# Kernel tuning notes

Measured on AMD Instinct MI355X. Metric: run time of the kernel, lower is better.

## Reference

```python
import jax, jax.numpy as jnp
import numpy as np

N = 50000        # nodes
E = 1_600_000    # edges
IN = 64          # in_channels
HID = 16         # hidden_dim (per-head channels)
HEADS = 8
OUT = 32         # out_channels
B = 256          # graphs in batch
NEG_SLOPE = 0.2  # PyG GATv2Conv default


def gatv2_conv(x, edge_index, wl, bl, wr, br, att, bias, heads, ch, concat, num_nodes):
    """Faithful GATv2Conv (PyG semantics, eval mode, add self-loops disabled upstream
    is not the case in PyG default, but the module uses default add_self_loops=True;
    we add them here)."""
    src, dst = edge_index[0], edge_index[1]
    # PyG default add_self_loops=True
    loop = jnp.arange(num_nodes, dtype=src.dtype)
    src = jnp.concatenate([src, loop])
    dst = jnp.concatenate([dst, loop])
    xl = (x @ wl + bl).reshape(num_nodes, heads, ch)  # source transform
    xr = (x @ wr + br).reshape(num_nodes, heads, ch)  # target transform
    # per-edge GATv2 score: att . leaky_relu(xl[src] + xr[dst])
    e = jax.nn.leaky_relu(xl[src] + xr[dst], NEG_SLOPE)          # [E, H, C]
    logits = jnp.einsum('ehc,hc->eh', e, att)                     # [E, H]
    # segment softmax over incoming edges of each dst node (max detached, as in PyG)
    m = jax.lax.stop_gradient(jax.ops.segment_max(logits, dst, num_segments=num_nodes))
    a = jnp.exp(logits - m[dst])
    denom = jax.ops.segment_sum(a, dst, num_segments=num_nodes)
    alpha = a / (denom[dst] + 1e-16)                              # [E, H]
    msg = xl[src] * alpha[..., None]                              # [E, H, C]
    out = jax.ops.segment_sum(msg, dst, num_segments=num_nodes)   # [N, H, C]
    if concat:
        out = out.reshape(num_nodes, heads * ch) + bias
    else:
        out = out.mean(axis=1) + bias
    return out


def global_mean_pool(x, batch, num_graphs):
    s = jax.ops.segment_sum(x, batch, num_segments=num_graphs)
    cnt = jax.ops.segment_sum(jnp.ones((x.shape[0],), x.dtype), batch, num_segments=num_graphs)
    return s / jnp.maximum(cnt, 1.0)[:, None]


def setup_inputs() -> dict:
    key = jax.random.key(0)
    ks = jax.random.split(key, 24)
    f32 = jnp.float32
    def g(k, shape, s=0.1):
        return jax.random.normal(k, shape, f32) * s
    inp = {
        'x': jax.random.normal(ks[0], (N, IN), f32),
        'edge_index': jax.random.randint(ks[1], (2, E), 0, N, dtype=jnp.int32),
        'batch': jnp.sort(jax.random.randint(ks[2], (N,), 0, B, dtype=jnp.int32)),
        # conv1: GATv2Conv(IN -> HID, heads=HEADS, concat=True)
        'wl1': g(ks[3], (IN, HEADS * HID)), 'bl1': jnp.zeros((HEADS * HID,), f32),
        'wr1': g(ks[4], (IN, HEADS * HID)), 'br1': jnp.zeros((HEADS * HID,), f32),
        'att1': g(ks[5], (HEADS, HID)),
        'bias1': jnp.zeros((HEADS * HID,), f32),
        # conv2: GATv2Conv(HEADS*HID -> HID, heads=1, concat=False)
        'wl2': g(ks[6], (HEADS * HID, HID)), 'bl2': jnp.zeros((HID,), f32),
        'wr2': g(ks[7], (HEADS * HID, HID)), 'br2': jnp.zeros((HID,), f32),
        'att2': g(ks[8], (1, HID)),
        'bias2': jnp.zeros((HID,), f32),
        # MLP: HID -> 2*HID -> HID -> OUT
        'w_m1': g(ks[9], (HID, 2 * HID)), 'b_m1': jnp.zeros((2 * HID,), f32),
        'w_m2': g(ks[10], (2 * HID, HID)), 'b_m2': jnp.zeros((HID,), f32),
        'w_m3': g(ks[11], (HID, OUT)), 'b_m3': jnp.zeros((OUT,), f32),
    }
    return inp


def reference(x, edge_index, batch,
              wl1, bl1, wr1, br1, att1, bias1,
              wl2, bl2, wr2, br2, att2, bias2,
              w_m1, b_m1, w_m2, b_m2, w_m3, b_m3):
    # eval mode: all dropouts are identity
    h = jax.nn.elu(gatv2_conv(x, edge_index, wl1, bl1, wr1, br1, att1, bias1,
                              HEADS, HID, True, N))
    h = jax.nn.elu(gatv2_conv(h, edge_index, wl2, bl2, wr2, br2, att2, bias2,
                              1, HID, False, N))
    h = global_mean_pool(h, batch, B)                 # [B, HID]
    h = jax.nn.elu(h @ w_m1 + b_m1)
    h = jax.nn.elu(h @ w_m2 + b_m2)
    return h @ w_m3 + b_m3                            # [B, OUT]
```

## Files before the change

kernel.cpp:

```cpp
#include <hip/hip_runtime.h>
#include <hip/hip_bf16.h>
#include <hip/hip_fp16.h>
#include <math.h>

#define NN   50000
#define NE   1600000
#define EP   (NE + NN)
#define NB   256
#define BK_SH 6
#define BKN  (1 << BK_SH)
#define NBKT ((NN + BKN - 1) >> BK_SH)
#define CAP_SH 12
#define CAP  (1 << CAP_SH)
#define ET   32
#define EB   (256 * ET)
#define EBLK ((NE + EB - 1) / EB)
#define G1   ((NN + 31) / 32)

__device__ __forceinline__ float elu_f(float x)   { return x > 0.0f ? x : expm1f(x); }
__device__ __forceinline__ float lrelu_f(float x) { return fmaxf(x, 0.2f * x); }

__global__ __launch_bounds__(256) void k_gemm1_bucket(
    const float* __restrict__ x, const float* __restrict__ wl,
    const float* __restrict__ bl, const float* __restrict__ wr,
    const float* __restrict__ br, __half* __restrict__ xl1, float* __restrict__ xr1,
    const int* __restrict__ ei, int* __restrict__ bcursor,
    unsigned int* __restrict__ bb)
{
    __shared__ float xs[32 * 64];
    __shared__ int lh[NBKT];
    __shared__ int cur[NBKT];
    const int tid = threadIdx.x;

    if (blockIdx.x < G1) {
        const int n0  = blockIdx.x * 32;
        const int nrem = min(32, NN - n0);

        const float4* xg = (const float4*)(x + (size_t)n0 * 64);
        float4* xs4 = (float4*)xs;
        const int lim4 = nrem * 16;
        for (int i = tid; i < lim4; i += 256) xs4[i] = xg[i];
        __syncthreads();

        const int g  = tid >> 6;
        const int c0 = (tid & 63) * 4;
        const bool isl = (c0 < 128);
        const float* w  = isl ? wl : wr;
        const float* b  = isl ? bl : br;
        const int    cw = isl ? c0 : (c0 - 128);

        float4 acc[8];
#pragma unroll
        for (int r = 0; r < 8; ++r) acc[r] = make_float4(0.f, 0.f, 0.f, 0.f);

        for (int k4 = 0; k4 < 16; ++k4) {
            const float4 w0 = *(const float4*)&w[(k4*4+0)*128 + cw];
            const float4 w1 = *(const float4*)&w[(k4*4+1)*128 + cw];
            const float4 w2 = *(const float4*)&w[(k4*4+2)*128 + cw];
            const float4 w3 = *(const float4*)&w[(k4*4+3)*128 + cw];
#pragma unroll
            for (int r = 0; r < 8; ++r) {
                const float4 xv = xs4[(g*8+r)*16 + k4];
                acc[r].x += xv.x*w0.x + xv.y*w1.x + xv.z*w2.x + xv.w*w3.x;
                acc[r].y += xv.x*w0.y + xv.y*w1.y + xv.z*w2.y + xv.w*w3.y;
                acc[r].z += xv.x*w0.z + xv.y*w1.z + xv.z*w2.z + xv.w*w3.z;
                acc[r].w += xv.x*w0.w + xv.y*w1.w + xv.z*w2.w + xv.w*w3.w;
            }
        }
        const float4 bv = *(const float4*)&b[cw];
#pragma unroll
        for (int r = 0; r < 8; ++r) {
            const int row = g*8 + r;
            if (row < nrem) {
                float4 o = make_float4(acc[r].x + bv.x, acc[r].y + bv.y,
                                       acc[r].z + bv.z, acc[r].w + bv.w);
                if (isl) {
                    __half2* dst = (__half2*)&xl1[(size_t)(n0 + row) * 128 + cw];
                    dst[0] = __floats2half2_rn(o.x, o.y);
                    dst[1] = __floats2half2_rn(o.z, o.w);
                } else {
                    *(float4*)&xr1[(size_t)(n0 + row) * 128 + cw] = o;
                }
            }
        }
    } else {
        const int bid = blockIdx.x - G1;
        for (int i = tid; i < NBKT; i += 256) lh[i] = 0;
        __syncthreads();

        const int t = bid * 256 + tid;
        const bool act = (t * ET < NE);
        int4 dreg[ET / 4];
        if (act) {
            const int4* dp = (const int4*)&ei[NE + t * ET];
#pragma unroll
            for (int q = 0; q < ET / 4; ++q) {
                dreg[q] = dp[q];
                atomicAdd(&lh[dreg[q].x >> BK_SH], 1);
                atomicAdd(&lh[dreg[q].y >> BK_SH], 1);
                atomicAdd(&lh[dreg[q].z >> BK_SH], 1);
                atomicAdd(&lh[dreg[q].w >> BK_SH], 1);
            }
        }
        __syncthreads();
        for (int i = tid; i < NBKT; i += 256) {
            int h = lh[i];
            if (h > 0) cur[i] = atomicAdd(&bcursor[i], h);
        }
        __syncthreads();
        if (act) {
            const int4* sp = (const int4*)&ei[t * ET];
#pragma unroll
            for (int q = 0; q < ET / 4; ++q) {
                int4 s = sp[q];
                int4 d = dreg[q];
                int bkt, p;
                bkt = d.x >> BK_SH; p = atomicAdd(&cur[bkt], 1);
                if (p < ((bkt + 1) << CAP_SH))
                    bb[p] = ((unsigned)(d.x & (BKN-1)) << 17) | (unsigned)s.x;
                bkt = d.y >> BK_SH; p = atomicAdd(&cur[bkt], 1);
                if (p < ((bkt + 1) << CAP_SH))
                    bb[p] = ((unsigned)(d.y & (BKN-1)) << 17) | (unsigned)s.y;
                bkt = d.z >> BK_SH; p = atomicAdd(&cur[bkt], 1);
                if (p < ((bkt + 1) << CAP_SH))
                    bb[p] = ((unsigned)(d.z & (BKN-1)) << 17) | (unsigned)s.z;
                bkt = d.w >> BK_SH; p = atomicAdd(&cur[bkt], 1);
                if (p < ((bkt + 1) << CAP_SH))
                    bb[p] = ((unsigned)(d.w & (BKN-1)) << 17) | (unsigned)s.w;
            }
        }
    }
}

__global__ void k_binit(int* __restrict__ bcursor)
{
    int i = blockIdx.x * 256 + threadIdx.x;
    if (i < NBKT) bcursor[i] = i << CAP_SH;
}

__global__ __launch_bounds__(256) void k_bfinal(
    const unsigned int* __restrict__ bb, const int* __restrict__ bcursor,
    int* __restrict__ rowp, int* __restrict__ slist)
{
    __shared__ int cnt[BKN], cur[BKN];
    __shared__ int red[256];
    const int b = blockIdx.x, tid = threadIdx.x;
    const int db0 = b << BK_SH;
    const int dn  = min(BKN, NN - db0);

    int part = 0;
    for (int i = tid; i < b; i += 256)
        part += min(bcursor[i] - (i << CAP_SH), CAP);
    red[tid] = part;
    __syncthreads();
    for (int ofs = 128; ofs >= 1; ofs >>= 1) {
        if (tid < ofs) red[tid] += red[tid + ofs];
        __syncthreads();
    }
    const int ebeg = red[0];
    const int count = min(bcursor[b] - (b << CAP_SH), CAP);
    const unsigned int* src = bb + ((size_t)b << CAP_SH);
    const int out0 = ebeg + db0;

    int c0 = 0;
    if (tid < BKN) {
        c0 = (tid < dn) ? 1 : 0;
        cnt[tid] = c0;
    }
    __syncthreads();
    for (int i = tid; i < count; i += 256)
        atomicAdd(&cnt[src[i] >> 17], 1);
    __syncthreads();
    if (tid < BKN) c0 = cnt[tid];
    for (int ofs = 1; ofs < BKN; ofs <<= 1) {
        int v = 0;
        if (tid < BKN && tid >= ofs) v = cnt[tid - ofs];
        __syncthreads();
        if (tid < BKN) cnt[tid] += v;
        __syncthreads();
    }
    if (tid < BKN) {
        int ex = cnt[tid] - c0;
        cur[tid] = ex + 1;
        if (tid < dn) {
            rowp[db0 + tid] = out0 + ex;
            slist[out0 + ex] = db0 + tid;
        }
    }
    if (b == 0 && tid == 0) rowp[NN] = EP;
    __syncthreads();
    for (int i = tid; i < count; i += 256) {
        unsigned u = src[i];
        int p = atomicAdd(&cur[u >> 17], 1);
        slist[out0 + p] = (int)(u & 0x1FFFFu);
    }
}

__global__ __launch_bounds__(256) void k_conv1_agg(
    const __half* __restrict__ xl1, const float* __restrict__ xr1,
    const float* __restrict__ att, const float* __restrict__ bias1,
    const int* __restrict__ rowp, const int* __restrict__ slist,
    float* __restrict__ h1)
{
    const int d = (blockIdx.x * 256 + threadIdx.x) >> 6;
    if (d >= NN) return;
    const int lane = threadIdx.x & 63;
    const int h = lane >> 3, e = lane & 7;
    const int cb = h * 16;

    float xrv[16], atv[16];
    {
        const float4* xrp = (const float4*)&xr1[(size_t)d * 128 + cb];
        const float4* atp = (const float4*)&att[cb];
#pragma unroll
        for (int q = 0; q < 4; ++q) {
            float4 a4 = xrp[q];
            xrv[q*4+0] = a4.x; xrv[q*4+1] = a4.y; xrv[q*4+2] = a4.z; xrv[q*4+3] = a4.w;
            float4 b4 = atp[q];
            atv[q*4+0] = b4.x; atv[q*4+1] = b4.y; atv[q*4+2] = b4.z; atv[q*4+3] = b4.w;
        }
    }

    const int beg = rowp[d], end = rowp[d + 1];

    float den = 0.f;
    float a[16];
#pragma unroll
    for (int c = 0; c < 16; ++c) a[c] = 0.f;

    for (int base = beg; base < end; base += 64) {
        const int nb = min(64, end - base);
        int sv = (lane < nb) ? slist[base + lane] : 0;
        for (int c8 = 0; c8 * 8 < nb; c8 += 2) {
            const int idx0 = c8 * 8 + e;
            const int idx1 = idx0 + 8;
            const int s0 = __shfl(sv, idx0);
            const int s1 = __shfl(sv, idx1 & 63);
            const bool e0 = (idx0 < nb), e1 = (idx1 < nb);
            float4 p0, p1, q0, q1;
            if (e0) {
                const float4* vp = (const float4*)(xl1 + (size_t)s0 * 128 + cb);
                p0 = vp[0]; p1 = vp[1];
            }
            if (e1) {
                const float4* vp = (const float4*)(xl1 + (size_t)s1 * 128 + cb);
                q0 = vp[0]; q1 = vp[1];
            }
            if (e0) {
                float v[16];
                const __half2* hh = (const __half2*)&p0;
#pragma unroll
                for (int q = 0; q < 4; ++q) {
                    float2 f = __half22float2(hh[q]);
                    v[2*q] = f.x; v[2*q+1] = f.y;
                }
                const __half2* hg = (const __half2*)&p1;
#pragma unroll
                for (int q = 0; q < 4; ++q) {
                    float2 f = __half22float2(hg[q]);
                    v[8+2*q] = f.x; v[9+2*q] = f.y;
                }
                float s = 0.f;
#pragma unroll
                for (int c = 0; c < 16; ++c) s += atv[c] * lrelu_f(v[c] + xrv[c]);
                const float w = __expf(fminf(s, 80.f));
                den += w;
#pragma unroll
                for (int c = 0; c < 16; ++c) a[c] += w * v[c];
            }
            if (e1) {
                float v[16];
                const __half2* hh = (const __half2*)&q0;
#pragma unroll
                for (int q = 0; q < 4; ++q) {
                    float2 f = __half22float2(hh[q]);
                    v[2*q] = f.x; v[2*q+1] = f.y;
                }
                const __half2* hg = (const __half2*)&q1;
#pragma unroll
                for (int q = 0; q < 4; ++q) {
                    float2 f = __half22float2(hg[q]);
                    v[8+2*q] = f.x; v[9+2*q] = f.y;
                }
                float s = 0.f;
#pragma unroll
                for (int c = 0; c < 16; ++c) s += atv[c] * lrelu_f(v[c] + xrv[c]);
                const float w = __expf(fminf(s, 80.f));
                den += w;
#pragma unroll
                for (int c = 0; c < 16; ++c) a[c] += w * v[c];
            }
        }
    }

    den += __shfl_xor(den, 1);
    den += __shfl_xor(den, 2);
    den += __shfl_xor(den, 4);

    const bool b0 = (e & 1), b1 = (e & 2), b2 = (e & 4);
    float t1[8], u1[8];
#pragma unroll
    for (int j = 0; j < 8; ++j) {
        t1[j] = b0 ? a[j + 8] : a[j];
        u1[j] = b0 ? a[j] : a[j + 8];
    }
#pragma unroll
    for (int j = 0; j < 8; ++j) t1[j] += __shfl_xor(u1[j], 1);
    float t2[4], u2[4];
#pragma unroll
    for (int j = 0; j < 4; ++j) {
        t2[j] = b1 ? t1[j + 4] : t1[j];
        u2[j] = b1 ? t1[j] : t1[j + 4];
    }
#pragma unroll
    for (int j = 0; j < 4; ++j) t2[j] += __shfl_xor(u2[j], 2);
    float t3[2], u3[2];
#pragma unroll
    for (int j = 0; j < 2; ++j) {
        t3[j] = b2 ? t2[j + 2] : t2[j];
        u3[j] = b2 ? t2[j] : t2[j + 2];
    }
#pragma unroll
    for (int j = 0; j < 2; ++j) t3[j] += __shfl_xor(u3[j], 4);

    const int c0 = (b0 ? 8 : 0) + (b1 ? 4 : 0) + (b2 ? 2 : 0);
    const float inv = 1.0f / (den + 1e-16f);
    const int c = cb + c0;
    const float o0 = elu_f(t3[0] * inv + bias1[c]);
    const float o1 = elu_f(t3[1] * inv + bias1[c + 1]);
    *(float2*)&h1[(size_t)d * 128 + c] = make_float2(o0, o1);
}

__global__ __launch_bounds__(256) void k_gemm2(
    const float* __restrict__ h1, const float* __restrict__ wl,
    const float* __restrict__ bl, const float* __restrict__ wr,
    const float* __restrict__ br, __half* __restrict__ xl2, float* __restrict__ xr2)
{
    __shared__ float xs[32 * 132];
    const int tid = threadIdx.x;
    const int n0  = blockIdx.x * 32;
    const int nrem = min(32, NN - n0);

    for (int i = tid; i < nrem * 128; i += 256) {
        int row = i >> 7, col = i & 127;
        xs[row * 132 + col] = h1[(size_t)(n0 + row) * 128 + col];
    }
    __syncthreads();

    const int r  = tid >> 3;
    const int c0 = (tid & 7) * 4;
    const bool isl = (c0 < 16);
    const float* w = isl ? wl : wr;
    const float* b = isl ? bl : br;
    const int    c = isl ? c0 : (c0 - 16);

    float4 acc = make_float4(0.f, 0.f, 0.f, 0.f);
    for (int k4 = 0; k4 < 32; ++k4) {
        const float4 w0 = *(const float4*)&w[(k4*4+0)*16 + c];
        const float4 w1 = *(const float4*)&w[(k4*4+1)*16 + c];
        const float4 w2 = *(const float4*)&w[(k4*4+2)*16 + c];
        const float4 w3 = *(const float4*)&w[(k4*4+3)*16 + c];
        const float4 xv = *(const float4*)&xs[r * 132 + k4 * 4];
        acc.x += xv.x*w0.x + xv.y*w1.x + xv.z*w2.x + xv.w*w3.x;
        acc.y += xv.x*w0.y + xv.y*w1.y + xv.z*w2.y + xv.w*w3.y;
        acc.z += xv.x*w0.z + xv.y*w1.z + xv.z*w2.z + xv.w*w3.z;
        acc.w += xv.x*w0.w + xv.y*w1.w + xv.z*w2.w + xv.w*w3.w;
    }
    if (r < nrem) {
        const float4 bv = *(const float4*)&b[c];
        float4 o = make_float4(acc.x + bv.x, acc.y + bv.y, acc.z + bv.z, acc.w + bv.w);
        if (isl) {
            __half2* dst = (__half2*)&xl2[(size_t)(n0 + r) * 16 + c];
            dst[0] = __floats2half2_rn(o.x, o.y);
            dst[1] = __floats2half2_rn(o.z, o.w);
        } else {
            *(float4*)&xr2[(size_t)(n0 + r) * 16 + c] = o;
        }
    }
}

__global__ __launch_bounds__(256) void k_conv2_agg(
    const __half* __restrict__ xl2, const float* __restrict__ xr2,
    const float* __restrict__ att, const float* __restrict__ bias2,
    const int* __restrict__ rowp, const int* __restrict__ slist,
    float* __restrict__ h2)
{
    const int d = (blockIdx.x * 256 + threadIdx.x) >> 6;
    if (d >= NN) return;
    const int lane = threadIdx.x & 63;
    const int eq = lane >> 2, c4 = lane & 3;

    const float4 xr = *(const float4*)&xr2[(size_t)d * 16 + c4 * 4];
    const float4 at = *(const float4*)&att[c4 * 4];
    const int beg = rowp[d], end = rowp[d + 1];

    float den = 0.f;
    float4 acc = make_float4(0.f, 0.f, 0.f, 0.f);

    for (int base = beg; base < end; base += 64) {
        const int nb = min(64, end - base);
        int sv = (lane < nb) ? slist[base + lane] : 0;
        for (int c16 = 0; c16 * 16 < nb; c16 += 2) {
            const int idx0 = c16 * 16 + eq;
            const int idx1 = idx0 + 16;
            const int s0 = __shfl(sv, idx0 & 63);
            const int s1 = __shfl(sv, idx1 & 63);
            const bool ee0 = (idx0 < nb), ee1 = (idx1 < nb);
            float2 ra, rb;
            if (ee0) ra = *(const float2*)(xl2 + (size_t)s0 * 16 + c4 * 4);
            if (ee1) rb = *(const float2*)(xl2 + (size_t)s1 * 16 + c4 * 4);
            {
                const __half2* hp = (const __half2*)&ra;
                float2 f0 = make_float2(0.f, 0.f), f1 = f0;
                if (ee0) { f0 = __half22float2(hp[0]); f1 = __half22float2(hp[1]); }
                float pp = at.x * lrelu_f(f0.x + xr.x)
                         + at.y * lrelu_f(f0.y + xr.y)
                         + at.z * lrelu_f(f1.x + xr.z)
                         + at.w * lrelu_f(f1.y + xr.w);
                pp += __shfl_xor(pp, 1);
                pp += __shfl_xor(pp, 2);
                if (ee0) {
                    const float w = __expf(fminf(pp, 80.f));
                    den += w;
                    acc.x += w * f0.x;
                    acc.y += w * f0.y;
                    acc.z += w * f1.x;
                    acc.w += w * f1.y;
                }
            }
            {
                const __half2* hp = (const __half2*)&rb;
                float2 f0 = make_float2(0.f, 0.f), f1 = f0;
                if (ee1) { f0 = __half22float2(hp[0]); f1 = __half22float2(hp[1]); }
                float pp = at.x * lrelu_f(f0.x + xr.x)
                         + at.y * lrelu_f(f0.y + xr.y)
                         + at.z * lrelu_f(f1.x + xr.z)
                         + at.w * lrelu_f(f1.y + xr.w);
                pp += __shfl_xor(pp, 1);
                pp += __shfl_xor(pp, 2);
                if (ee1) {
                    const float w = __expf(fminf(pp, 80.f));
                    den += w;
                    acc.x += w * f0.x;
                    acc.y += w * f0.y;
                    acc.z += w * f1.x;
                    acc.w += w * f1.y;
                }
            }
        }
    }
#pragma unroll
    for (int ofs = 4; ofs < 64; ofs <<= 1) {
        den   += __shfl_xor(den, ofs);
        acc.x += __shfl_xor(acc.x, ofs);
        acc.y += __shfl_xor(acc.y, ofs);
        acc.z += __shfl_xor(acc.z, ofs);
        acc.w += __shfl_xor(acc.w, ofs);
    }
    if (eq == 0) {
        const float inv = 1.0f / (den + 1e-16f);
        const float4 bv = *(const float4*)&bias2[c4 * 4];
        float4 o;
        o.x = elu_f(acc.x * inv + bv.x);
        o.y = elu_f(acc.y * inv + bv.y);
        o.z = elu_f(acc.z * inv + bv.z);
        o.w = elu_f(acc.w * inv + bv.w);
        *(float4*)&h2[(size_t)d * 16 + c4 * 4] = o;
    }
}

__global__ __launch_bounds__(256) void k_pool(
    const float* __restrict__ h2, const int* __restrict__ batch,
    float* __restrict__ pooled, float* __restrict__ cnt)
{
    __shared__ int se[2];
    __shared__ float sm[256];
    const int b = blockIdx.x, tid = threadIdx.x;
    if (tid < 2) {
        int key = b + tid, lo = 0, hi = NN;
        while (lo < hi) {
            int mid = (lo + hi) >> 1;
            if (batch[mid] < key) lo = mid + 1; else hi = mid;
        }
        se[tid] = lo;
    }
    __syncthreads();
    const int s = se[0], e = se[1];
    const int c = tid & 15, slot = tid >> 4;
    float acc = 0.f;
    for (int n = s + slot; n < e; n += 16) acc += h2[(size_t)n * 16 + c];
    sm[tid] = acc;
    __syncthreads();
    for (int ofs = 128; ofs >= 16; ofs >>= 1) {
        if (tid < ofs) sm[tid] += sm[tid + ofs];
        __syncthreads();
    }
    if (tid < 16) pooled[b * 16 + tid] = sm[tid];
    if (tid == 16) cnt[b] = (float)(e - s);
}

__global__ __launch_bounds__(256) void k_mlp(
    const float* __restrict__ pooled, const float* __restrict__ cnt,
    const float* __restrict__ w1, const float* __restrict__ b1,
    const float* __restrict__ w2, const float* __restrict__ b2,
    const float* __restrict__ w3, const float* __restrict__ b3,
    float* __restrict__ out)
{
    __shared__ float w1s[16*32], w2s[32*16], w3s[16*32], b1s[32], b2s[16], b3s[32];
    const int tid = threadIdx.x;
    for (int i = tid; i < 512; i += 256) { w1s[i] = w1[i]; w2s[i] = w2[i]; w3s[i] = w3[i]; }
    if (tid < 32) b1s[tid] = b1[tid];
    if (tid < 16) b2s[tid] = b2[tid];
    if (tid < 32) b3s[tid] = b3[tid];
    __syncthreads();

    const int g = tid;
    const float inv = 1.0f / fmaxf(cnt[g], 1.0f);
    float hb[16];
#pragma unroll
    for (int k = 0; k < 16; ++k) hb[k] = pooled[g * 16 + k] * inv;

    float t1[32];
#pragma unroll
    for (int j = 0; j < 32; ++j) t1[j] = b1s[j];
    for (int k = 0; k < 16; ++k)
#pragma unroll
        for (int j = 0; j < 32; ++j) t1[j] += hb[k] * w1s[k * 32 + j];
#pragma unroll
    for (int j = 0; j < 32; ++j) t1[j] = elu_f(t1[j]);

    float t2[16];
#pragma unroll
    for (int j = 0; j < 16; ++j) t2[j] = b2s[j];
    for (int k = 0; k < 32; ++k)
#pragma unroll
        for (int j = 0; j < 16; ++j) t2[j] += t1[k] * w2s[k * 16 + j];
#pragma unroll
    for (int j = 0; j < 16; ++j) t2[j] = elu_f(t2[j]);

#pragma unroll
    for (int j = 0; j < 32; ++j) {
        float o = b3s[j];
        for (int k = 0; k < 16; ++k) o += t2[k] * w3s[k * 32 + j];
        out[g * 32 + j] = o;
    }
}

extern "C" void kernel_launch(void* const* d_in, const int* in_sizes, int n_in,
                              void* d_out, int out_size, void* d_ws, size_t ws_size,
                              hipStream_t stream)
{
    const float* x     = (const float*)d_in[0];
    const int*   ei    = (const int*)d_in[1];
    const int*   batch = (const int*)d_in[2];
    const float* wl1   = (const float*)d_in[3];
    const float* bl1   = (const float*)d_in[4];
    const float* wr1   = (const float*)d_in[5];
    const float* br1   = (const float*)d_in[6];
    const float* att1  = (const float*)d_in[7];
    const float* bias1 = (const float*)d_in[8];
    const float* wl2   = (const float*)d_in[9];
    const float* bl2   = (const float*)d_in[10];
    const float* wr2   = (const float*)d_in[11];
    const float* br2   = (const float*)d_in[12];
    const float* att2  = (const float*)d_in[13];
    const float* bias2 = (const float*)d_in[14];
    const float* wm1   = (const float*)d_in[15];
    const float* bm1   = (const float*)d_in[16];
    const float* wm2   = (const float*)d_in[17];
    const float* bm2   = (const float*)d_in[18];
    const float* wm3   = (const float*)d_in[19];
    const float* bm3   = (const float*)d_in[20];
    float* out = (float*)d_out;

    char* base = (char*)d_ws;
    size_t off = 0;
    auto alloc = [&](size_t bytes) -> void* {
        void* p = base + off;
        off += (bytes + 255) & ~(size_t)255;
        return p;
    };
    __half* xl1  = (__half*)alloc((size_t)NN * 128 * 2);
    float* xr1   = (float*)alloc((size_t)NN * 128 * 4);
    float* h1    = (float*)alloc((size_t)NN * 128 * 4);
    int*   slist = (int*)  alloc((size_t)EP * 4);
    unsigned int* bb = (unsigned int*)alloc((size_t)NBKT * CAP * 4);
    int*   rowp  = (int*)  alloc((size_t)(NN + 1) * 4);
    int*   bcursor=(int*)  alloc((size_t)NBKT * 4);
    __half* xl2  = (__half*)alloc((size_t)NN * 16 * 2);
    float* xr2   = (float*)alloc((size_t)NN * 16 * 4);
    float* h2    = (float*)alloc((size_t)NN * 16 * 4);
    float* pooled= (float*)alloc((size_t)NB * 16 * 4);
    float* cnt   = (float*)alloc((size_t)NB * 4);

    k_binit<<<(NBKT + 255) / 256, 256, 0, stream>>>(bcursor);
    k_gemm1_bucket<<<G1 + EBLK, 256, 0, stream>>>(x, wl1, bl1, wr1, br1, xl1, xr1,
                                                  ei, bcursor, bb);
    k_bfinal<<<NBKT, 256, 0, stream>>>(bb, bcursor, rowp, slist);
    k_conv1_agg<<<(NN * 64) / 256, 256, 0, stream>>>(xl1, xr1, att1, bias1, rowp, slist, h1);
    k_gemm2<<<(NN + 31) / 32, 256, 0, stream>>>(h1, wl2, bl2, wr2, br2, xl2, xr2);
    k_conv2_agg<<<(NN * 64) / 256, 256, 0, stream>>>(xl2, xr2, att2, bias2, rowp, slist, h2);
    k_pool<<<NB, 256, 0, stream>>>(h2, batch, pooled, cnt);
    k_mlp<<<1, 256, 0, stream>>>(pooled, cnt, wm1, bm1, wm2, bm2, wm3, bm3, out);
}
```

Before: 324.5 us.

## Fuse layer-2 linear transform into conv1 aggregation and simplify conv2 loop

Folds the second GATv2 layer's linear projections (wl2/wr2) into the conv1 aggregation kernel. Each block stages the combined 128x32 weight in shared memory and computes xl2/xr2 directly from the per-node h1 row kept in LDS. This removes the h1 buffer's global write and read-back and one kernel launch. The cost is a 16KB weight load into LDS per block (each block handles only 4 nodes) plus extra syncthreads, and the dropped `d >= NN` early return is harmless only because NN*64 divides evenly by 256. Separately, conv2's edge loop is de-unrolled from two edges per iteration to one, which may reduce memory-level parallelism.

```diff
diff --git a/kernel.cpp b/kernel.cpp
--- a/kernel.cpp
+++ b/kernel.cpp
@@ -200,11 +200,25 @@
     const __half* __restrict__ xl1, const float* __restrict__ xr1,
     const float* __restrict__ att, const float* __restrict__ bias1,
     const int* __restrict__ rowp, const int* __restrict__ slist,
-    float* __restrict__ h1)
-{
-    const int d = (blockIdx.x * 256 + threadIdx.x) >> 6;
-    if (d >= NN) return;
-    const int lane = threadIdx.x & 63;
+    const float* __restrict__ wl2, const float* __restrict__ bl2,
+    const float* __restrict__ wr2, const float* __restrict__ br2,
+    __half* __restrict__ xl2, float* __restrict__ xr2)
+{
+    __shared__ float wcomb[128 * 32];
+    __shared__ float bcomb[32];
+    __shared__ float h1rows[4 * 128];
+    const int tid = threadIdx.x;
+
+    for (int i = tid; i < 2048; i += 256) {
+        const int cc = i >> 4, jj = i & 15;
+        wcomb[cc * 32 + jj]      = wl2[i];
+        wcomb[cc * 32 + 16 + jj] = wr2[i];
+    }
+    if (tid < 16) { bcomb[tid] = bl2[tid]; bcomb[16 + tid] = br2[tid]; }
+    __syncthreads();
+
+    const int d = (blockIdx.x * 256 + tid) >> 6;
+    const int lane = tid & 63;
     const int h = lane >> 3, e = lane & 7;
     const int cb = h * 16;
 
@@ -328,53 +342,24 @@
     const int c = cb + c0;
     const float o0 = elu_f(t3[0] * inv + bias1[c]);
     const float o1 = elu_f(t3[1] * inv + bias1[c + 1]);
-    *(float2*)&h1[(size_t)d * 128 + c] = make_float2(o0, o1);
-}
-
-__global__ __launch_bounds__(256) void k_gemm2(
-    const float* __restrict__ h1, const float* __restrict__ wl,
-    const float* __restrict__ bl, const float* __restrict__ wr,
-    const float* __restrict__ br, __half* __restrict__ xl2, float* __restrict__ xr2)
-{
-    __shared__ float xs[32 * 132];
-    const int tid = threadIdx.x;
-    const int n0  = blockIdx.x * 32;
-    const int nrem = min(32, NN - n0);
-
-    for (int i = tid; i < nrem * 128; i += 256) {
-        int row = i >> 7, col = i & 127;
-        xs[row * 132 + col] = h1[(size_t)(n0 + row) * 128 + col];
-    }
-    __syncthreads();
-
-    const int r  = tid >> 3;
-    const int c0 = (tid & 7) * 4;
-    const bool isl = (c0 < 16);
-    const float* w = isl ? wl : wr;
-    const float* b = isl ? bl : br;
-    const int    c = isl ? c0 : (c0 - 16);
-
-    float4 acc = make_float4(0.f, 0.f, 0.f, 0.f);
-    for (int k4 = 0; k4 < 32; ++k4) {
-        const float4 w0 = *(const float4*)&w[(k4*4+0)*16 + c];
-        const float4 w1 = *(const float4*)&w[(k4*4+1)*16 + c];
-        const float4 w2 = *(const float4*)&w[(k4*4+2)*16 + c];
-        const float4 w3 = *(const float4*)&w[(k4*4+3)*16 + c];
-        const float4 xv = *(const float4*)&xs[r * 132 + k4 * 4];
-        acc.x += xv.x*w0.x + xv.y*w1.x + xv.z*w2.x + xv.w*w3.x;
-        acc.y += xv.x*w0.y + xv.y*w1.y + xv.z*w2.y + xv.w*w3.y;
-        acc.z += xv.x*w0.z + xv.y*w1.z + xv.z*w2.z + xv.w*w3.z;
-        acc.w += xv.x*w0.w + xv.y*w1.w + xv.z*w2.w + xv.w*w3.w;
-    }
-    if (r < nrem) {
-        const float4 bv = *(const float4*)&b[c];
-        float4 o = make_float4(acc.x + bv.x, acc.y + bv.y, acc.z + bv.z, acc.w + bv.w);
-        if (isl) {
-            __half2* dst = (__half2*)&xl2[(size_t)(n0 + r) * 16 + c];
-            dst[0] = __floats2half2_rn(o.x, o.y);
-            dst[1] = __floats2half2_rn(o.z, o.w);
-        } else {
-            *(float4*)&xr2[(size_t)(n0 + r) * 16 + c] = o;
+
+    const int wv = tid >> 6;
+    h1rows[wv * 128 + c]     = o0;
+    h1rows[wv * 128 + c + 1] = o1;
+    __syncthreads();
+    {
+        const int j = lane & 31;
+        const int half = lane >> 5;
+        const float* hr = &h1rows[wv * 128 + half * 64];
+        const float* wc = &wcomb[(half * 64) * 32 + j];
+        float sum = 0.f;
+#pragma unroll 8
+        for (int cc = 0; cc < 64; ++cc) sum += hr[cc] * wc[cc * 32];
+        sum += __shfl_xor(sum, 32);
+        if (half == 0) {
+            sum += bcomb[j];
+            if (j < 16) xl2[(size_t)d * 16 + j] = __float2half(sum);
+            else        xr2[(size_t)d * 16 + (j - 16)] = sum;
         }
     }
 }
@@ -400,52 +385,25 @@
     for (int base = beg; base < end; base += 64) {
         const int nb = min(64, end - base);
         int sv = (lane < nb) ? slist[base + lane] : 0;
-        for (int c16 = 0; c16 * 16 < nb; c16 += 2) {
-            const int idx0 = c16 * 16 + eq;
-            const int idx1 = idx0 + 16;
-            const int s0 = __shfl(sv, idx0 & 63);
-            const int s1 = __shfl(sv, idx1 & 63);
-            const bool ee0 = (idx0 < nb), ee1 = (idx1 < nb);
-            float2 ra, rb;
-            if (ee0) ra = *(const float2*)(xl2 + (size_t)s0 * 16 + c4 * 4);
-            if (ee1) rb = *(const float2*)(xl2 + (size_t)s1 * 16 + c4 * 4);
-            {
-                const __half2* hp = (const __half2*)&ra;
-                float2 f0 = make_float2(0.f, 0.f), f1 = f0;
-                if (ee0) { f0 = __half22float2(hp[0]); f1 = __half22float2(hp[1]); }
+        for (int c16 = 0; c16 * 16 < nb; ++c16) {
+            const int idx = c16 * 16 + eq;
+            const int src = __shfl(sv, idx & 63);
+            if (idx < nb) {
+                const __half2* hp = (const __half2*)(xl2 + (size_t)src * 16 + c4 * 4);
+                const float2 f0 = __half22float2(hp[0]);
+                const float2 f1 = __half22float2(hp[1]);
                 float pp = at.x * lrelu_f(f0.x + xr.x)
                          + at.y * lrelu_f(f0.y + xr.y)
                          + at.z * lrelu_f(f1.x + xr.z)
                          + at.w * lrelu_f(f1.y + xr.w);
                 pp += __shfl_xor(pp, 1);
                 pp += __shfl_xor(pp, 2);
-                if (ee0) {
-                    const float w = __expf(fminf(pp, 80.f));
-                    den += w;
-                    acc.x += w * f0.x;
-                    acc.y += w * f0.y;
-                    acc.z += w * f1.x;
-                    acc.w += w * f1.y;
-                }
-            }
-            {
-                const __half2* hp = (const __half2*)&rb;
-                float2 f0 = make_float2(0.f, 0.f), f1 = f0;
-                if (ee1) { f0 = __half22float2(hp[0]); f1 = __half22float2(hp[1]); }
-                float pp = at.x * lrelu_f(f0.x + xr.x)
-                         + at.y * lrelu_f(f0.y + xr.y)
-                         + at.z * lrelu_f(f1.x + xr.z)
-                         + at.w * lrelu_f(f1.y + xr.w);
-                pp += __shfl_xor(pp, 1);
-                pp += __shfl_xor(pp, 2);
-                if (ee1) {
-                    const float w = __expf(fminf(pp, 80.f));
-                    den += w;
-                    acc.x += w * f0.x;
-                    acc.y += w * f0.y;
-                    acc.z += w * f1.x;
-                    acc.w += w * f1.y;
-                }
+                const float w = __expf(fminf(pp, 80.f));
+                den += w;
+                acc.x += w * f0.x;
+                acc.y += w * f0.y;
+                acc.z += w * f1.x;
+                acc.w += w * f1.y;
             }
         }
     }
@@ -582,7 +540,6 @@
     };
     __half* xl1  = (__half*)alloc((size_t)NN * 128 * 2);
     float* xr1   = (float*)alloc((size_t)NN * 128 * 4);
-    float* h1    = (float*)alloc((size_t)NN * 128 * 4);
     int*   slist = (int*)  alloc((size_t)EP * 4);
     unsigned int* bb = (unsigned int*)alloc((size_t)NBKT * CAP * 4);
     int*   rowp  = (int*)  alloc((size_t)(NN + 1) * 4);
@@ -597,8 +554,8 @@
     k_gemm1_bucket<<<G1 + EBLK, 256, 0, stream>>>(x, wl1, bl1, wr1, br1, xl1, xr1,
                                                   ei, bcursor, bb);
     k_bfinal<<<NBKT, 256, 0, stream>>>(bb, bcursor, rowp, slist);
-    k_conv1_agg<<<(NN * 64) / 256, 256, 0, stream>>>(xl1, xr1, att1, bias1, rowp, slist, h1);
-    k_gemm2<<<(NN + 31) / 32, 256, 0, stream>>>(h1, wl2, bl2, wr2, br2, xl2, xr2);
+    k_conv1_agg<<<(NN * 64) / 256, 256, 0, stream>>>(xl1, xr1, att1, bias1, rowp, slist,
+                                                     wl2, bl2, wr2, br2, xl2, xr2);
     k_conv2_agg<<<(NN * 64) / 256, 256, 0, stream>>>(xl2, xr2, att2, bias2, rowp, slist, h2);
     k_pool<<<NB, 256, 0, stream>>>(h2, batch, pooled, cnt);
     k_mlp<<<1, 256, 0, stream>>>(pooled, cnt, wm1, bm1, wm2, bm2, wm3, bm3, out);
```

Measured after the change: 321.3 us. About the same (-1.0%).
